# Optimization experiments

Hardware: AMD Instinct MI355X
Metric: run time of the kernel (lower is better)

Reference implementation:

```python
import jax, jax.numpy as jnp
import numpy as np

D_IN = 1024
D_OUT = 1024
SEQ = 2048
BATCH = 4


def setup_inputs() -> dict:
    key = jax.random.key(0)
    k_x, k_q, k_k, k_v = jax.random.split(key, 4)
    scale = 1.0 / np.sqrt(D_IN)  # ~ torch Linear init scale
    x = jax.random.normal(k_x, (BATCH, SEQ, D_IN), dtype=jnp.float32)
    # torch nn.Linear weights have shape [d_out, d_in]; y = x @ W.T
    Wq = jax.random.uniform(k_q, (D_OUT, D_IN), jnp.float32, -scale, scale)
    Wk = jax.random.uniform(k_k, (D_OUT, D_IN), jnp.float32, -scale, scale)
    Wv = jax.random.uniform(k_v, (D_OUT, D_IN), jnp.float32, -scale, scale)
    return {"x": x, "Wq": Wq, "Wk": Wk, "Wv": Wv}


def reference(x, Wq, Wk, Wv):
    # projections (no bias, qkv_bias=False)
    q = jnp.einsum("bsd,ed->bse", x, Wq)  # [B,S,D_OUT]
    k = jnp.einsum("bsd,ed->bse", x, Wk)
    v = jnp.einsum("bsd,ed->bse", x, Wv)
    scores = jnp.einsum("bqe,bke->bqk", q, k)  # [B,S,S]
    seq = scores.shape[-1]
    causal = jnp.tril(jnp.ones((seq, seq), dtype=bool))  # keep lower-tri
    scores = jnp.where(causal[None], scores, -jnp.inf)
    # note: original scales AFTER masking: softmax(scores / sqrt(d_k))
    inv_sqrt_dk = 1.0 / np.sqrt(k.shape[-1]).astype(np.float32)
    weights = jax.nn.softmax(scores * inv_sqrt_dk, axis=-1)
    # dropout p=0.0 (eval-equivalent): identity
    return jnp.einsum("bqk,bke->bqe", weights, v)
```

## Files before the change

kernel.cpp:

```cpp
#include <hip/hip_runtime.h>
#include <hip/hip_bf16.h>

typedef __bf16 v8bf __attribute__((ext_vector_type(8)));
typedef float v4f __attribute__((ext_vector_type(4)));

#define GBL_AS(p) ((const __attribute__((address_space(1))) unsigned int*)(p))
#define LDS_AS(p) ((__attribute__((address_space(3))) unsigned int*)(p))

#define WAIT_VM4() __builtin_amdgcn_s_waitcnt(0x0F74)
#define WAIT_VM0() __builtin_amdgcn_s_waitcnt(0x0F70)

__global__ void cast_f32_bf16(const float* __restrict__ src,
                              __hip_bfloat16* __restrict__ dst, int n) {
  int i = (blockIdx.x * 256 + threadIdx.x) * 4;
  if (i >= n) return;
  float4 f = *(const float4*)(src + i);
  union { __hip_bfloat16 h[4]; uint2 u; } pk;
  pk.h[0] = __float2bfloat16(f.x);
  pk.h[1] = __float2bfloat16(f.y);
  pk.h[2] = __float2bfloat16(f.z);
  pk.h[3] = __float2bfloat16(f.w);
  *(uint2*)(dst + i) = pk.u;
}

__global__ void cast_w3(const float* __restrict__ a, const float* __restrict__ b,
                        const float* __restrict__ c, __hip_bfloat16* __restrict__ dst) {
  int seg = blockIdx.x >> 10;
  const float* src = seg == 0 ? a : (seg == 1 ? b : c);
  int i = ((blockIdx.x & 1023) * 256 + threadIdx.x) * 4;
  float4 f = *(const float4*)(src + i);
  union { __hip_bfloat16 h[4]; uint2 u; } pk;
  pk.h[0] = __float2bfloat16(f.x);
  pk.h[1] = __float2bfloat16(f.y);
  pk.h[2] = __float2bfloat16(f.z);
  pk.h[3] = __float2bfloat16(f.w);
  *(uint2*)(dst + seg * 1048576 + i) = pk.u;
}

template<int MODE>
__global__ __launch_bounds__(256, 3)
void gemm_nt(const __hip_bfloat16* __restrict__ A, long sAb, int lda,
             const __hip_bfloat16* __restrict__ B, long sBb, int ldb,
             void* __restrict__ Cv, long sCb, int ldc,
             int K, float scale, float* __restrict__ sums,
             __hip_bfloat16* __restrict__ vTp) {
  const int tid = threadIdx.x;
  const int l = tid & 63, w = tid >> 6;
  int z, nb, mb, kend = K;
  if (MODE == 0) {
    z = blockIdx.x >> 3; nb = (blockIdx.x & 7) << 7; mb = blockIdx.y << 7;
  } else if (MODE == 1) {
    const int id = blockIdx.x;
    z = id & 3;
    const int t = id >> 2;
    int m = (int)((__builtin_sqrtf(8.0f * t + 1.0f) - 1.0f) * 0.5f);
    while ((m + 1) * (m + 2) / 2 <= t) ++m;
    while (m * (m + 1) / 2 > t) --m;
    mb = m << 7;
    nb = (t - m * (m + 1) / 2) << 7;
  } else {
    const int id = blockIdx.x;
    const int half = id >> 8, r8 = id & 255;
    const int m = r8 >> 4, low = r8 & 15;
    nb = (low >> 1) << 7;
    z = (half << 1) | (low & 1);
    const int mi = half ? (15 - m) : m;
    mb = mi << 7;
    kend = (mi + 1) << 7;
  }

  A += (long)z * sAb;
  B += (long)z * sBb;

  __shared__ alignas(16) __hip_bfloat16 As[3][128 * 32];
  __shared__ alignas(16) __hip_bfloat16 Bs[3][128 * 32];

  v4f acc[4][4] = {};
  const int wm = (w >> 1) * 64, wn = (w & 1) * 64;

  const int cb0 = w * 64;
  const int q0 = cb0 + l, r0s = q0 >> 2;
  const int c0s = ((q0 & 3) ^ ((r0s >> 1) & 3)) << 3;
  const int cb1 = 256 + w * 64;
  const int q1 = cb1 + l, r1s = q1 >> 2;
  const int c1s = ((q1 & 3) ^ ((r1s >> 1) & 3)) << 3;

  const __hip_bfloat16* Arow0 = A + (long)(mb + r0s) * lda + c0s;
  const __hip_bfloat16* Arow1 = A + (long)(mb + r1s) * lda + c1s;
  const __hip_bfloat16* Brow0 = B + (long)(nb + r0s) * ldb + c0s;
  const __hip_bfloat16* Brow1 = B + (long)(nb + r1s) * ldb + c1s;

  const int arow = wm + (l & 15);
  const int ldsA = arow * 32 + ((((l >> 4) ^ ((arow >> 1) & 3))) << 3);
  const int brow = wn + (l & 15);
  const int ldsB = brow * 32 + ((((l >> 4) ^ ((brow >> 1) & 3))) << 3);

#define STAGE_T(K0, BUF) do {                                                   \
    __builtin_amdgcn_global_load_lds(GBL_AS(Arow0 + (K0)),                      \
        LDS_AS(&As[BUF][cb0 * 8]), 16, 0, 0);                                   \
    __builtin_amdgcn_global_load_lds(GBL_AS(Brow0 + (K0)),                      \
        LDS_AS(&Bs[BUF][cb0 * 8]), 16, 0, 0);                                   \
    __builtin_amdgcn_global_load_lds(GBL_AS(Arow1 + (K0)),                      \
        LDS_AS(&As[BUF][cb1 * 8]), 16, 0, 0);                                   \
    __builtin_amdgcn_global_load_lds(GBL_AS(Brow1 + (K0)),                      \
        LDS_AS(&Bs[BUF][cb1 * 8]), 16, 0, 0);                                   \
  } while (0)

#define COMPUTE(BI) do {                                                        \
    v8bf af[4], bfr[4];                                                         \
    _Pragma("unroll")                                                           \
    for (int i = 0; i < 4; ++i) {                                               \
      af[i]  = *(const v8bf*)(&As[BI][ldsA + i * 512]);                         \
      bfr[i] = *(const v8bf*)(&Bs[BI][ldsB + i * 512]);                         \
    }                                                                           \
    _Pragma("unroll")                                                           \
    for (int i = 0; i < 4; ++i)                                                 \
      _Pragma("unroll")                                                         \
      for (int j = 0; j < 4; ++j)                                               \
        acc[i][j] = __builtin_amdgcn_mfma_f32_16x16x32_bf16(af[i], bfr[j],      \
                                                            acc[i][j], 0, 0, 0);\
  } while (0)

#define KITER(IT) do {                                                          \
    if constexpr ((IT) < 31) WAIT_VM4(); else WAIT_VM0();                       \
    __builtin_amdgcn_s_barrier();                                               \
    if constexpr ((IT) < 30) STAGE_T((IT) * 32 + 64, ((IT) + 2) % 3);           \
    COMPUTE((IT) % 3);                                                          \
  } while (0)

  if constexpr (MODE == 0 || MODE == 1) {
    STAGE_T(0, 0);
    STAGE_T(32, 1);
    KITER(0);  KITER(1);  KITER(2);  KITER(3);  KITER(4);  KITER(5);  KITER(6);
    KITER(7);  KITER(8);  KITER(9);  KITER(10); KITER(11); KITER(12); KITER(13);
    KITER(14); KITER(15); KITER(16); KITER(17); KITER(18); KITER(19); KITER(20);
    KITER(21); KITER(22); KITER(23); KITER(24); KITER(25); KITER(26); KITER(27);
    KITER(28); KITER(29); KITER(30); KITER(31);
  } else {
    auto stage = [&](int k0, int buf) {
      __builtin_amdgcn_global_load_lds(GBL_AS(Arow0 + k0),
          LDS_AS(&As[buf][cb0 * 8]), 16, 0, 0);
      __builtin_amdgcn_global_load_lds(GBL_AS(Brow0 + k0),
          LDS_AS(&Bs[buf][cb0 * 8]), 16, 0, 0);
      __builtin_amdgcn_global_load_lds(GBL_AS(Arow1 + k0),
          LDS_AS(&As[buf][cb1 * 8]), 16, 0, 0);
      __builtin_amdgcn_global_load_lds(GBL_AS(Brow1 + k0),
          LDS_AS(&Bs[buf][cb1 * 8]), 16, 0, 0);
    };
    stage(0, 0);
    if (32 < kend) stage(32, 1);
    int bi = 0;
    for (int k0 = 0; k0 < kend; k0 += 32) {
      if (k0 + 32 < kend) WAIT_VM4(); else WAIT_VM0();
      __builtin_amdgcn_s_barrier();
      if (k0 + 64 < kend) stage(k0 + 64, bi == 0 ? 2 : bi - 1);
      v8bf af[4], bfr[4];
#pragma unroll
      for (int i = 0; i < 4; ++i) {
        af[i]  = *(const v8bf*)(&As[bi][ldsA + i * 512]);
        bfr[i] = *(const v8bf*)(&Bs[bi][ldsB + i * 512]);
      }
#pragma unroll
      for (int i = 0; i < 4; ++i)
#pragma unroll
        for (int j = 0; j < 4; ++j)
          acc[i][j] = __builtin_amdgcn_mfma_f32_16x16x32_bf16(af[i], bfr[j], acc[i][j], 0, 0, 0);
      bi = (bi == 2) ? 0 : bi + 1;
    }
  }
#undef KITER
#undef COMPUTE
#undef STAGE_T

  const int col0 = nb + wn + (l & 15);
  const int row0 = mb + wm + ((l >> 4) << 2);
  if constexpr (MODE == 0) {
    if (z < 2) {
      __hip_bfloat16* C = (__hip_bfloat16*)Cv + (long)z * sCb;
#pragma unroll
      for (int i = 0; i < 4; ++i)
#pragma unroll
        for (int r = 0; r < 4; ++r) {
          long ro = (long)(row0 + i * 16 + r) * ldc;
#pragma unroll
          for (int j = 0; j < 4; ++j)
            C[ro + col0 + j * 16] = __float2bfloat16(acc[i][j][r] * scale);
        }
    } else {
      const long b = row0 >> 11;
      const int seq0 = row0 & 2047;
#pragma unroll
      for (int i = 0; i < 4; ++i)
#pragma unroll
        for (int j = 0; j < 4; ++j) {
          union { __hip_bfloat16 h[4]; uint2 u; } pk;
#pragma unroll
          for (int r = 0; r < 4; ++r) pk.h[r] = __float2bfloat16(acc[i][j][r]);
          *(uint2*)(vTp + b * 2097152 + (long)(col0 + j * 16) * 2048 +
                    (seq0 + i * 16)) = pk.u;
        }
    }
  } else if constexpr (MODE == 1) {
    __hip_bfloat16* C = (__hip_bfloat16*)Cv + (long)z * sCb;
    float* srow = sums + z * 2048;
#pragma unroll
    for (int i = 0; i < 4; ++i)
#pragma unroll
      for (int r = 0; r < 4; ++r) {
        const int m = row0 + i * 16 + r;
        long ro = (long)m * ldc;
        float sp = 0.f;
#pragma unroll
        for (int j = 0; j < 4; ++j) {
          const int n = col0 + j * 16;
          float p = (n <= m) ? __expf(acc[i][j][r] * scale) : 0.0f;
          sp += p;
          C[ro + n] = __float2bfloat16(p);
        }
        sp += __shfl_xor(sp, 1);
        sp += __shfl_xor(sp, 2);
        sp += __shfl_xor(sp, 4);
        sp += __shfl_xor(sp, 8);
        if ((l & 15) == 0) atomicAdd(&srow[m], sp);
      }
  } else {
    float* C = (float*)Cv + (long)z * sCb;
    const float* srow = sums + z * 2048;
#pragma unroll
    for (int i = 0; i < 4; ++i)
#pragma unroll
      for (int r = 0; r < 4; ++r) {
        const int m = row0 + i * 16 + r;
        const float s = 1.0f / srow[m];
        long ro = (long)m * ldc;
#pragma unroll
        for (int j = 0; j < 4; ++j)
          C[ro + col0 + j * 16] = acc[i][j][r] * s;
      }
  }
}

extern "C" void kernel_launch(void* const* d_in, const int* in_sizes, int n_in,
                              void* d_out, int out_size, void* d_ws, size_t ws_size,
                              hipStream_t stream) {
  const float* x  = (const float*)d_in[0];
  const float* Wq = (const float*)d_in[1];
  const float* Wk = (const float*)d_in[2];
  const float* Wv = (const float*)d_in[3];
  float* out = (float*)d_out;
  char* ws = (char*)d_ws;

  __hip_bfloat16* qkv = (__hip_bfloat16*)ws;
  __hip_bfloat16* vT  = (__hip_bfloat16*)(ws + 50331648);
  __hip_bfloat16* xb  = (__hip_bfloat16*)(ws + 67108864);
  __hip_bfloat16* Wb  = (__hip_bfloat16*)(ws + 83886080);
  __hip_bfloat16* P   = (__hip_bfloat16*)(ws + 67108864);
  float* sums         = (float*)(ws + 100663296);

  hipMemsetAsync(sums, 0, 8192 * sizeof(float), stream);

  cast_f32_bf16<<<8192, 256, 0, stream>>>(x, xb, 8388608);
  cast_w3<<<3072, 256, 0, stream>>>(Wq, Wk, Wv, Wb);

  gemm_nt<0><<<dim3(24, 64, 1), 256, 0, stream>>>(
      xb, 0L, 1024, Wb, 1048576L, 1024, qkv, 8388608L, 1024,
      1024, 1.0f, nullptr, vT);

  gemm_nt<1><<<dim3(544, 1, 1), 256, 0, stream>>>(
      qkv, 2097152L, 1024, qkv + 8388608, 2097152L, 1024,
      P, 4194304L, 2048, 1024, 0.03125f, sums, nullptr);

  gemm_nt<2><<<dim3(512, 1, 1), 256, 0, stream>>>(
      P, 4194304L, 2048, vT, 2097152L, 2048,
      out, 2097152L, 1024, 2048, 1.0f, sums, nullptr);
}
```

Baseline: 232.4 us.

## Move all three GEMMs to 256x256 tiles with 8-wave ping-pong pipeline

Replaces the 128x128, 4-wave, triple-buffered GEMM with a 256x256-tile, 8-wave (512-thread) kernel using a 64-wide K step, double buffering, staggered loads and s_setprio around MFMA phases. The score grid becomes a triangular schedule over 256 tiles. The PV stage splits long causal K ranges into two segments that are combined with float atomics, which requires zeroing the output first. The aim is more data reuse per load and better MFMA utilisation. The cost is fewer blocks (144 for scores), fewer resident waves per CU, an extra memset, and atomic traffic in PV.

```diff
diff --git a/kernel.cpp b/kernel.cpp
--- a/kernel.cpp
+++ b/kernel.cpp
@@ -7,8 +7,9 @@
 #define GBL_AS(p) ((const __attribute__((address_space(1))) unsigned int*)(p))
 #define LDS_AS(p) ((__attribute__((address_space(3))) unsigned int*)(p))
 
-#define WAIT_VM4() __builtin_amdgcn_s_waitcnt(0x0F74)
+#define WAIT_VM6() __builtin_amdgcn_s_waitcnt(0x0F76)
 #define WAIT_VM0() __builtin_amdgcn_s_waitcnt(0x0F70)
+#define BAR() __builtin_amdgcn_s_barrier()
 
 __global__ void cast_f32_bf16(const float* __restrict__ src,
                               __hip_bfloat16* __restrict__ dst, int n) {
@@ -38,177 +39,180 @@
 }
 
 template<int MODE>
-__global__ __launch_bounds__(256, 3)
-void gemm_nt(const __hip_bfloat16* __restrict__ A, long sAb, int lda,
-             const __hip_bfloat16* __restrict__ B, long sBb, int ldb,
-             void* __restrict__ Cv, long sCb, int ldc,
-             int K, float scale, float* __restrict__ sums,
-             __hip_bfloat16* __restrict__ vTp) {
+__device__ static __forceinline__
+void gemm8_body(const __hip_bfloat16* __restrict__ A, long sAb, int lda,
+                const __hip_bfloat16* __restrict__ B, long sBb, int ldb,
+                void* __restrict__ Cv, long sCb, int ldc,
+                float scale, float* __restrict__ sums,
+                __hip_bfloat16* __restrict__ vTp) {
   const int tid = threadIdx.x;
   const int l = tid & 63, w = tid >> 6;
-  int z, nb, mb, kend = K;
+  const int wr = w >> 2, wc = w & 3;
+
+  int z, mb, nb, k0 = 0, NT;
+  bool atom = false;
   if (MODE == 0) {
-    z = blockIdx.x >> 3; nb = (blockIdx.x & 7) << 7; mb = blockIdx.y << 7;
+    const int id = blockIdx.x;
+    z = id >> 7; mb = ((id >> 2) & 31) << 8; nb = (id & 3) << 8;
+    NT = 16;
   } else if (MODE == 1) {
     const int id = blockIdx.x;
-    z = id & 3;
-    const int t = id >> 2;
+    z = id / 36;
+    const int t = id - z * 36;
     int m = (int)((__builtin_sqrtf(8.0f * t + 1.0f) - 1.0f) * 0.5f);
     while ((m + 1) * (m + 2) / 2 <= t) ++m;
     while (m * (m + 1) / 2 > t) --m;
-    mb = m << 7;
-    nb = (t - m * (m + 1) / 2) << 7;
+    mb = m << 8; nb = (t - m * (m + 1) / 2) << 8;
+    NT = 16;
   } else {
     const int id = blockIdx.x;
-    const int half = id >> 8, r8 = id & 255;
-    const int m = r8 >> 4, low = r8 & 15;
-    nb = (low >> 1) << 7;
-    z = (half << 1) | (low & 1);
-    const int mi = half ? (15 - m) : m;
-    mb = mi << 7;
-    kend = (mi + 1) << 7;
+    z = id / 48;
+    const int r48 = id - z * 48;
+    const int c = r48 / 12, s = r48 - c * 12;
+    nb = c << 8;
+    int i, seg;
+    if (s < 4) { i = s; seg = 0; }
+    else       { i = 4 + ((s - 4) >> 1); seg = (s - 4) & 1; }
+    mb = i << 8;
+    k0 = seg ? 1024 : 0;
+    const int k1 = seg ? ((i + 1) << 8) : ((i < 4) ? ((i + 1) << 8) : 1024);
+    NT = (k1 - k0) >> 6;
+    atom = (i >= 4);
   }
 
-  A += (long)z * sAb;
-  B += (long)z * sBb;
-
-  __shared__ alignas(16) __hip_bfloat16 As[3][128 * 32];
-  __shared__ alignas(16) __hip_bfloat16 Bs[3][128 * 32];
-
-  v4f acc[4][4] = {};
-  const int wm = (w >> 1) * 64, wn = (w & 1) * 64;
-
-  const int cb0 = w * 64;
-  const int q0 = cb0 + l, r0s = q0 >> 2;
-  const int c0s = ((q0 & 3) ^ ((r0s >> 1) & 3)) << 3;
-  const int cb1 = 256 + w * 64;
-  const int q1 = cb1 + l, r1s = q1 >> 2;
-  const int c1s = ((q1 & 3) ^ ((r1s >> 1) & 3)) << 3;
-
-  const __hip_bfloat16* Arow0 = A + (long)(mb + r0s) * lda + c0s;
-  const __hip_bfloat16* Arow1 = A + (long)(mb + r1s) * lda + c1s;
-  const __hip_bfloat16* Brow0 = B + (long)(nb + r0s) * ldb + c0s;
-  const __hip_bfloat16* Brow1 = B + (long)(nb + r1s) * ldb + c1s;
-
-  const int arow = wm + (l & 15);
-  const int ldsA = arow * 32 + ((((l >> 4) ^ ((arow >> 1) & 3))) << 3);
-  const int brow = wn + (l & 15);
-  const int ldsB = brow * 32 + ((((l >> 4) ^ ((brow >> 1) & 3))) << 3);
-
-#define STAGE_T(K0, BUF) do {                                                   \
-    __builtin_amdgcn_global_load_lds(GBL_AS(Arow0 + (K0)),                      \
-        LDS_AS(&As[BUF][cb0 * 8]), 16, 0, 0);                                   \
-    __builtin_amdgcn_global_load_lds(GBL_AS(Brow0 + (K0)),                      \
-        LDS_AS(&Bs[BUF][cb0 * 8]), 16, 0, 0);                                   \
-    __builtin_amdgcn_global_load_lds(GBL_AS(Arow1 + (K0)),                      \
-        LDS_AS(&As[BUF][cb1 * 8]), 16, 0, 0);                                   \
-    __builtin_amdgcn_global_load_lds(GBL_AS(Brow1 + (K0)),                      \
-        LDS_AS(&Bs[BUF][cb1 * 8]), 16, 0, 0);                                   \
-  } while (0)
-
-#define COMPUTE(BI) do {                                                        \
-    v8bf af[4], bfr[4];                                                         \
-    _Pragma("unroll")                                                           \
-    for (int i = 0; i < 4; ++i) {                                               \
-      af[i]  = *(const v8bf*)(&As[BI][ldsA + i * 512]);                         \
-      bfr[i] = *(const v8bf*)(&Bs[BI][ldsB + i * 512]);                         \
-    }                                                                           \
-    _Pragma("unroll")                                                           \
-    for (int i = 0; i < 4; ++i)                                                 \
-      _Pragma("unroll")                                                         \
-      for (int j = 0; j < 4; ++j)                                               \
-        acc[i][j] = __builtin_amdgcn_mfma_f32_16x16x32_bf16(af[i], bfr[j],      \
-                                                            acc[i][j], 0, 0, 0);\
-  } while (0)
-
-#define KITER(IT) do {                                                          \
-    if constexpr ((IT) < 31) WAIT_VM4(); else WAIT_VM0();                       \
-    __builtin_amdgcn_s_barrier();                                               \
-    if constexpr ((IT) < 30) STAGE_T((IT) * 32 + 64, ((IT) + 2) % 3);           \
-    COMPUTE((IT) % 3);                                                          \
-  } while (0)
-
-  if constexpr (MODE == 0 || MODE == 1) {
-    STAGE_T(0, 0);
-    STAGE_T(32, 1);
-    KITER(0);  KITER(1);  KITER(2);  KITER(3);  KITER(4);  KITER(5);  KITER(6);
-    KITER(7);  KITER(8);  KITER(9);  KITER(10); KITER(11); KITER(12); KITER(13);
-    KITER(14); KITER(15); KITER(16); KITER(17); KITER(18); KITER(19); KITER(20);
-    KITER(21); KITER(22); KITER(23); KITER(24); KITER(25); KITER(26); KITER(27);
-    KITER(28); KITER(29); KITER(30); KITER(31);
-  } else {
-    auto stage = [&](int k0, int buf) {
-      __builtin_amdgcn_global_load_lds(GBL_AS(Arow0 + k0),
-          LDS_AS(&As[buf][cb0 * 8]), 16, 0, 0);
-      __builtin_amdgcn_global_load_lds(GBL_AS(Brow0 + k0),
-          LDS_AS(&Bs[buf][cb0 * 8]), 16, 0, 0);
-      __builtin_amdgcn_global_load_lds(GBL_AS(Arow1 + k0),
-          LDS_AS(&As[buf][cb1 * 8]), 16, 0, 0);
-      __builtin_amdgcn_global_load_lds(GBL_AS(Brow1 + k0),
-          LDS_AS(&Bs[buf][cb1 * 8]), 16, 0, 0);
-    };
-    stage(0, 0);
-    if (32 < kend) stage(32, 1);
-    int bi = 0;
-    for (int k0 = 0; k0 < kend; k0 += 32) {
-      if (k0 + 32 < kend) WAIT_VM4(); else WAIT_VM0();
-      __builtin_amdgcn_s_barrier();
-      if (k0 + 64 < kend) stage(k0 + 64, bi == 0 ? 2 : bi - 1);
-      v8bf af[4], bfr[4];
-#pragma unroll
-      for (int i = 0; i < 4; ++i) {
-        af[i]  = *(const v8bf*)(&As[bi][ldsA + i * 512]);
-        bfr[i] = *(const v8bf*)(&Bs[bi][ldsB + i * 512]);
-      }
-#pragma unroll
-      for (int i = 0; i < 4; ++i)
-#pragma unroll
-        for (int j = 0; j < 4; ++j)
-          acc[i][j] = __builtin_amdgcn_mfma_f32_16x16x32_bf16(af[i], bfr[j], acc[i][j], 0, 0, 0);
-      bi = (bi == 2) ? 0 : bi + 1;
-    }
+  A += (long)z * sAb + k0;
+  B += (long)z * sBb + k0;
+
+  __shared__ alignas(16) __hip_bfloat16 As[2][256 * 64];
+  __shared__ alignas(16) __hip_bfloat16 Bs[2][256 * 64];
+
+  v4f acc[8][4] = {};
+
+  const int srow = w * 8 + (l >> 3);
+  const int scol = (((l & 7) ^ ((l >> 3) & 7)) << 3);
+  const __hip_bfloat16* gA = A + (long)(mb + srow) * lda + scol;
+  const __hip_bfloat16* gB = B + (long)(nb + srow) * ldb + scol;
+  const long qA = 64L * lda, qB = 64L * ldb;
+  const int ldst = w * 512;
+
+#define STA(QI, T, BUF) __builtin_amdgcn_global_load_lds(                      \
+    GBL_AS(gA + (QI) * qA + (T) * 64), LDS_AS(&As[BUF][(QI) * 4096 + ldst]),   \
+    16, 0, 0)
+#define STB(QI, T, BUF) __builtin_amdgcn_global_load_lds(                      \
+    GBL_AS(gB + (QI) * qB + (T) * 64), LDS_AS(&Bs[BUF][(QI) * 4096 + ldst]),   \
+    16, 0, 0)
+#define SIX(T, BUF) do { STB(0,T,BUF); STB(1,T,BUF); STB(2,T,BUF);             \
+                         STB(3,T,BUF); STA(0,T,BUF); STA(2,T,BUF); } while (0)
+#define TWO(T, BUF) do { STA(1,T,BUF); STA(3,T,BUF); } while (0)
+
+  const int ldsA0 = (wr * 128 + (l & 15)) * 64;
+  const int ldsB0 = (wc * 64 + (l & 15)) * 64;
+  const int csw0 = (((l >> 4) ^ (l & 7)) << 3);
+  const int csw1 = csw0 ^ 32;
+
+  SIX(0, 0);
+  TWO(0, 0);
+  if (NT > 1) { SIX(1, 1); WAIT_VM6(); } else { WAIT_VM0(); }
+  BAR();
+
+  for (int t = 0; t < NT; ++t) {
+    const int b = t & 1;
+    const __hip_bfloat16* Ab = As[b];
+    const __hip_bfloat16* Bb = Bs[b];
+    v8bf a0[4], a1[4], b0[4], b1[4];
+    if (t + 1 < NT) TWO(t + 1, (t + 1) & 1);
+#pragma unroll
+    for (int i = 0; i < 4; ++i) a0[i] = *(const v8bf*)(Ab + ldsA0 + i * 1024 + csw0);
+#pragma unroll
+    for (int j = 0; j < 4; ++j) b0[j] = *(const v8bf*)(Bb + ldsB0 + j * 1024 + csw0);
+    BAR();
+    __builtin_amdgcn_s_setprio(1);
+#pragma unroll
+    for (int i = 0; i < 4; ++i)
+#pragma unroll
+      for (int j = 0; j < 4; ++j)
+        acc[i][j] = __builtin_amdgcn_mfma_f32_16x16x32_bf16(a0[i], b0[j], acc[i][j], 0, 0, 0);
+    __builtin_amdgcn_s_setprio(0);
+    BAR();
+#pragma unroll
+    for (int i = 0; i < 4; ++i) a1[i] = *(const v8bf*)(Ab + ldsA0 + (i + 4) * 1024 + csw0);
+    BAR();
+    __builtin_amdgcn_s_setprio(1);
+#pragma unroll
+    for (int i = 0; i < 4; ++i)
+#pragma unroll
+      for (int j = 0; j < 4; ++j)
+        acc[i + 4][j] = __builtin_amdgcn_mfma_f32_16x16x32_bf16(a1[i], b0[j], acc[i + 4][j], 0, 0, 0);
+    __builtin_amdgcn_s_setprio(0);
+    BAR();
+#pragma unroll
+    for (int i = 0; i < 4; ++i) a0[i] = *(const v8bf*)(Ab + ldsA0 + i * 1024 + csw1);
+#pragma unroll
+    for (int j = 0; j < 4; ++j) b1[j] = *(const v8bf*)(Bb + ldsB0 + j * 1024 + csw1);
+    BAR();
+    __builtin_amdgcn_s_setprio(1);
+#pragma unroll
+    for (int i = 0; i < 4; ++i)
+#pragma unroll
+      for (int j = 0; j < 4; ++j)
+        acc[i][j] = __builtin_amdgcn_mfma_f32_16x16x32_bf16(a0[i], b1[j], acc[i][j], 0, 0, 0);
+    __builtin_amdgcn_s_setprio(0);
+    BAR();
+    if (t + 2 < NT) SIX(t + 2, b);
+#pragma unroll
+    for (int i = 0; i < 4; ++i) a1[i] = *(const v8bf*)(Ab + ldsA0 + (i + 4) * 1024 + csw1);
+    if (t + 2 < NT) WAIT_VM6(); else WAIT_VM0();
+    BAR();
+    __builtin_amdgcn_s_setprio(1);
+#pragma unroll
+    for (int i = 0; i < 4; ++i)
+#pragma unroll
+      for (int j = 0; j < 4; ++j)
+        acc[i + 4][j] = __builtin_amdgcn_mfma_f32_16x16x32_bf16(a1[i], b1[j], acc[i + 4][j], 0, 0, 0);
+    __builtin_amdgcn_s_setprio(0);
+    BAR();
   }
-#undef KITER
-#undef COMPUTE
-#undef STAGE_T
-
-  const int col0 = nb + wn + (l & 15);
-  const int row0 = mb + wm + ((l >> 4) << 2);
+#undef SIX
+#undef TWO
+#undef STA
+#undef STB
+
+  const int col0 = nb + wc * 64 + (l & 15);
+  const int row0 = mb + wr * 128 + ((l >> 4) << 2);
   if constexpr (MODE == 0) {
     if (z < 2) {
       __hip_bfloat16* C = (__hip_bfloat16*)Cv + (long)z * sCb;
 #pragma unroll
-      for (int i = 0; i < 4; ++i)
+      for (int i = 0; i < 8; ++i)
 #pragma unroll
         for (int r = 0; r < 4; ++r) {
-          long ro = (long)(row0 + i * 16 + r) * ldc;
+          const long ro = (long)(row0 + i * 16 + r) * ldc;
 #pragma unroll
           for (int j = 0; j < 4; ++j)
             C[ro + col0 + j * 16] = __float2bfloat16(acc[i][j][r] * scale);
         }
     } else {
-      const long b = row0 >> 11;
+      const long bb = (long)(row0 >> 11) * 2097152;
       const int seq0 = row0 & 2047;
 #pragma unroll
-      for (int i = 0; i < 4; ++i)
+      for (int i = 0; i < 8; ++i)
 #pragma unroll
         for (int j = 0; j < 4; ++j) {
           union { __hip_bfloat16 h[4]; uint2 u; } pk;
 #pragma unroll
           for (int r = 0; r < 4; ++r) pk.h[r] = __float2bfloat16(acc[i][j][r]);
-          *(uint2*)(vTp + b * 2097152 + (long)(col0 + j * 16) * 2048 +
-                    (seq0 + i * 16)) = pk.u;
+          *(uint2*)(vTp + bb + (long)(col0 + j * 16) * 2048 + seq0 + i * 16) = pk.u;
         }
     }
   } else if constexpr (MODE == 1) {
     __hip_bfloat16* C = (__hip_bfloat16*)Cv + (long)z * sCb;
     float* srow = sums + z * 2048;
 #pragma unroll
-    for (int i = 0; i < 4; ++i)
+    for (int i = 0; i < 8; ++i)
 #pragma unroll
       for (int r = 0; r < 4; ++r) {
         const int m = row0 + i * 16 + r;
-        long ro = (long)m * ldc;
+        const long ro = (long)m * ldc;
         float sp = 0.f;
 #pragma unroll
         for (int j = 0; j < 4; ++j) {
@@ -227,17 +231,47 @@
     float* C = (float*)Cv + (long)z * sCb;
     const float* srow = sums + z * 2048;
 #pragma unroll
-    for (int i = 0; i < 4; ++i)
+    for (int i = 0; i < 8; ++i)
 #pragma unroll
       for (int r = 0; r < 4; ++r) {
         const int m = row0 + i * 16 + r;
-        const float s = 1.0f / srow[m];
-        long ro = (long)m * ldc;
-#pragma unroll
-        for (int j = 0; j < 4; ++j)
-          C[ro + col0 + j * 16] = acc[i][j][r] * s;
+        const float sc = 1.0f / srow[m];
+        const long ro = (long)m * ldc;
+#pragma unroll
+        for (int j = 0; j < 4; ++j) {
+          const float v = acc[i][j][r] * sc;
+          if (atom) atomicAdd(&C[ro + col0 + j * 16], v);
+          else C[ro + col0 + j * 16] = v;
+        }
       }
   }
+}
+
+__global__ __launch_bounds__(512, 2)
+void proj8(const __hip_bfloat16* __restrict__ A, long sAb, int lda,
+           const __hip_bfloat16* __restrict__ B, long sBb, int ldb,
+           void* __restrict__ Cv, long sCb, int ldc,
+           float scale, float* __restrict__ sums,
+           __hip_bfloat16* __restrict__ vTp) {
+  gemm8_body<0>(A, sAb, lda, B, sBb, ldb, Cv, sCb, ldc, scale, sums, vTp);
+}
+
+__global__ __launch_bounds__(512, 2)
+void score8(const __hip_bfloat16* __restrict__ A, long sAb, int lda,
+            const __hip_bfloat16* __restrict__ B, long sBb, int ldb,
+            void* __restrict__ Cv, long sCb, int ldc,
+            float scale, float* __restrict__ sums,
+            __hip_bfloat16* __restrict__ vTp) {
+  gemm8_body<1>(A, sAb, lda, B, sBb, ldb, Cv, sCb, ldc, scale, sums, vTp);
+}
+
+__global__ __launch_bounds__(512, 2)
+void pv8(const __hip_bfloat16* __restrict__ A, long sAb, int lda,
+         const __hip_bfloat16* __restrict__ B, long sBb, int ldb,
+         void* __restrict__ Cv, long sCb, int ldc,
+         float scale, float* __restrict__ sums,
+         __hip_bfloat16* __restrict__ vTp) {
+  gemm8_body<2>(A, sAb, lda, B, sBb, ldb, Cv, sCb, ldc, scale, sums, vTp);
 }
 
 extern "C" void kernel_launch(void* const* d_in, const int* in_sizes, int n_in,
@@ -258,19 +292,20 @@
   float* sums         = (float*)(ws + 100663296);
 
   hipMemsetAsync(sums, 0, 8192 * sizeof(float), stream);
+  hipMemsetAsync(out, 0, 33554432, stream);
 
   cast_f32_bf16<<<8192, 256, 0, stream>>>(x, xb, 8388608);
   cast_w3<<<3072, 256, 0, stream>>>(Wq, Wk, Wv, Wb);
 
-  gemm_nt<0><<<dim3(24, 64, 1), 256, 0, stream>>>(
+  proj8<<<dim3(384, 1, 1), 512, 0, stream>>>(
       xb, 0L, 1024, Wb, 1048576L, 1024, qkv, 8388608L, 1024,
-      1024, 1.0f, nullptr, vT);
-
-  gemm_nt<1><<<dim3(544, 1, 1), 256, 0, stream>>>(
+      1.0f, nullptr, vT);
+
+  score8<<<dim3(144, 1, 1), 512, 0, stream>>>(
       qkv, 2097152L, 1024, qkv + 8388608, 2097152L, 1024,
-      P, 4194304L, 2048, 1024, 0.03125f, sums, nullptr);
-
-  gemm_nt<2><<<dim3(512, 1, 1), 256, 0, stream>>>(
+      P, 4194304L, 2048, 0.03125f, sums, nullptr);
+
+  pv8<<<dim3(192, 1, 1), 512, 0, stream>>>(
       P, 4194304L, 2048, vT, 2097152L, 2048,
-      out, 2097152L, 1024, 2048, 1.0f, sums, nullptr);
-}
+      out, 2097152L, 1024, 1.0f, sums, nullptr);
+}
```

After: 303.1 us. 1.3x slower.
